# Optimization experiments

Hardware: AMD Instinct MI355X
Metric: run time of the kernel (lower is better)

Reference implementation:

```python
import jax, jax.numpy as jnp
import numpy as np

NUM_EXPERTS = 64
TOP_K = 8
NUM_TOKENS = 8192
HIDDEN = 1024
INTER = 512


def setup_inputs() -> dict:
    key = jax.random.key(0)
    k1, k2, k3, k4 = jax.random.split(key, 4)
    # 0.02 scale keeps activations in a sane range (randn weights with fan-in 1024)
    return {
        "hidden_states": jax.random.normal(k1, (NUM_TOKENS, HIDDEN), jnp.float32),
        "router_weight": jax.random.normal(k2, (HIDDEN, NUM_EXPERTS), jnp.float32) * 0.02,
        "merged_gate_up_proj": jax.random.normal(k3, (NUM_EXPERTS, HIDDEN, 2 * INTER), jnp.float32) * 0.02,
        "merged_down_proj": jax.random.normal(k4, (NUM_EXPERTS, INTER, HIDDEN), jnp.float32) * 0.02,
    }


def reference(hidden_states, router_weight, merged_gate_up_proj, merged_down_proj):
    T, H = hidden_states.shape
    E = router_weight.shape[1]

    # ---- Router: softmax over experts, top-k, renormalize top-k weights ----
    logits = hidden_states @ router_weight                       # [T, E]
    probs = jax.nn.softmax(logits, axis=-1)
    routing_weights, routing_indices = jax.lax.top_k(probs, TOP_K)  # [T, k]
    routing_weights = routing_weights / routing_weights.sum(-1, keepdims=True)

    # ---- Permute (haojun_permute_topk): replicate tokens topk times, stable-sort by expert ----
    flat_indices = routing_indices.reshape(-1)                   # [T*k]
    sort_order = jnp.argsort(flat_indices)                       # stable sort
    flat_states = jnp.repeat(hidden_states, TOP_K, axis=0)       # [T*k, H]
    permuted = flat_states[sort_order]                           # tokens grouped by expert
    group_sizes = jnp.bincount(flat_indices, length=E).astype(jnp.int32)  # tokens per expert

    # ---- Grouped MLP (grouped_gemm.gmm equivalent): y_i = x_i @ W[expert(i)] ----
    merged = jax.lax.ragged_dot(permuted, merged_gate_up_proj, group_sizes)  # [T*k, 2*I]
    gate, up = jnp.split(merged, 2, axis=-1)
    h = jax.nn.silu(gate) * up                                   # SiLU-gated (hidden_act='silu')
    expert_out = jax.lax.ragged_dot(h, merged_down_proj, group_sizes)        # [T*k, H]

    # ---- Unpermute: invert the sort, weight by routing probs, sum over top-k ----
    inv = jnp.argsort(sort_order)                                # unsort_order
    unpermuted = expert_out[inv].reshape(T, TOP_K, H)
    return (unpermuted * routing_weights[..., None]).sum(axis=1)  # [T, H]
```

## Files before the change

### kernel.cpp

```cpp
#include <hip/hip_runtime.h>
#include <cstdint>
#include <cstddef>

typedef __bf16 bf16_t;
typedef __bf16 bf16x8 __attribute__((ext_vector_type(8)));
typedef __bf16 bf16x4 __attribute__((ext_vector_type(4)));
typedef float f32x4 __attribute__((ext_vector_type(4)));

#define T_TOKENS 8192
#define HID 1024
#define INTER 512
#define NEXP 64
#define TOPK 8
#define NROWS (T_TOKENS * TOPK)
#define RT_TOK 16

typedef const unsigned int __attribute__((address_space(1)))* gptr_t;
typedef unsigned int __attribute__((address_space(3)))* lptr_t;

__device__ __forceinline__ void gload_lds16(const void* g, void* l) {
  __builtin_amdgcn_global_load_lds((gptr_t)g, (lptr_t)l, 16, 0, 0);
}

__device__ __forceinline__ f32x4 mfma16(bf16x8 a, bf16x8 b, f32x4 c) {
  return __builtin_amdgcn_mfma_f32_16x16x32_bf16(a, b, c, 0, 0, 0);
}

__device__ __forceinline__ int xcd_swizzle(int bid, int nwg) {
  int q = nwg >> 3;
  int xcd = bid & 7, i = bid >> 3;
  return xcd * q + i;
}

__global__ void transpose_cvt2_kernel(const float* __restrict__ w1, bf16_t* __restrict__ Wt1,
                                      const float* __restrict__ w2, bf16_t* __restrict__ Wt2,
                                      int* __restrict__ cntz) {
  const int tid = threadIdx.x;
  if (blockIdx.x == 0 && blockIdx.y == 0 && blockIdx.z == 0 && tid < 128) cntz[tid] = 0;

  const int e = blockIdx.z;
  const float* W; bf16_t* Wt; int K, k0;
  if (blockIdx.y < 16) {
    W = w1; Wt = Wt1; K = 1024; k0 = blockIdx.y * 64;
  } else {
    W = w2; Wt = Wt2; K = 512; k0 = (blockIdx.y - 16) * 64;
  }
  const int N = 1024;
  const int n0 = blockIdx.x * 64;

  __shared__ bf16_t tile[64][65];
  {
    const int r = tid >> 2, cq = tid & 3;
    const float* src = W + ((size_t)e * K + k0 + r) * N + n0 + cq * 16;
#pragma unroll
    for (int q = 0; q < 4; ++q) {
      float4 v = *(const float4*)(src + q * 4);
      tile[r][cq * 16 + q * 4 + 0] = (bf16_t)v.x;
      tile[r][cq * 16 + q * 4 + 1] = (bf16_t)v.y;
      tile[r][cq * 16 + q * 4 + 2] = (bf16_t)v.z;
      tile[r][cq * 16 + q * 4 + 3] = (bf16_t)v.w;
    }
  }
  __syncthreads();
  {
    const int nl = tid >> 2, kq = tid & 3;
    __align__(16) bf16_t tmp[16];
#pragma unroll
    for (int i = 0; i < 16; ++i) tmp[i] = tile[kq * 16 + i][nl];
    bf16_t* dst = Wt + ((size_t)e * N + n0 + nl) * K + k0 + kq * 16;
    *(bf16x8*)(dst + 0) = *(const bf16x8*)(tmp + 0);
    *(bf16x8*)(dst + 8) = *(const bf16x8*)(tmp + 8);
  }
}

__launch_bounds__(256, 2)
__global__ void router_kernel(const float* __restrict__ hs, const float* __restrict__ rw,
                              float* __restrict__ wval, int* __restrict__ widx,
                              bf16_t* __restrict__ hb) {
  const int t0 = blockIdx.x * RT_TOK;
  const int tid = threadIdx.x;
  const int lane = tid & 63, w = tid >> 6;
  __shared__ float hsl[RT_TOK][HID / 4][4];
  __shared__ float part[4][RT_TOK][NEXP];

  for (int i = tid; i < RT_TOK * (HID / 4); i += 256) {
    int t = i >> 8, c = i & 255;
    float4 v = ((const float4*)(hs + (size_t)(t0 + t) * HID))[c];
    *(float4*)&hsl[t][c][0] = v;
    bf16x4 o;
    o[0] = (bf16_t)v.x; o[1] = (bf16_t)v.y; o[2] = (bf16_t)v.z; o[3] = (bf16_t)v.w;
    *(bf16x4*)(hb + (size_t)(t0 + t) * HID + c * 4) = o;
  }
  __syncthreads();

  float acc[RT_TOK];
#pragma unroll
  for (int t = 0; t < RT_TOK; ++t) acc[t] = 0.f;
  const int kb = w * 256;
  for (int kc = 0; kc < 64; ++kc) {
    const int k = kb + kc * 4;
    float r0 = rw[(size_t)(k + 0) * NEXP + lane];
    float r1 = rw[(size_t)(k + 1) * NEXP + lane];
    float r2 = rw[(size_t)(k + 2) * NEXP + lane];
    float r3 = rw[(size_t)(k + 3) * NEXP + lane];
#pragma unroll
    for (int t = 0; t < RT_TOK; ++t) {
      float4 hv = *(const float4*)&hsl[t][(kb >> 2) + kc][0];
      acc[t] = fmaf(hv.x, r0, acc[t]);
      acc[t] = fmaf(hv.y, r1, acc[t]);
      acc[t] = fmaf(hv.z, r2, acc[t]);
      acc[t] = fmaf(hv.w, r3, acc[t]);
    }
  }
#pragma unroll
  for (int t = 0; t < RT_TOK; ++t) part[w][t][lane] = acc[t];
  __syncthreads();

  for (int j = 0; j < 4; ++j) {
    const int t = w * 4 + j;
    float logit = part[0][t][lane] + part[1][t][lane] + part[2][t][lane] + part[3][t][lane];
    float m = logit;
    for (int off = 32; off; off >>= 1) m = fmaxf(m, __shfl_xor(m, off));
    float ex = expf(logit - m);
    float Z = ex;
    for (int off = 32; off; off >>= 1) Z += __shfl_xor(Z, off);
    float p = ex / Z;
    float sum8 = 0.f;
    float outv[8]; int outi[8];
#pragma unroll
    for (int s = 0; s < 8; ++s) {
      float v = p; int idx = lane;
      for (int off = 32; off; off >>= 1) {
        float vv = __shfl_xor(v, off);
        int ii = __shfl_xor(idx, off);
        if (vv > v || (vv == v && ii < idx)) { v = vv; idx = ii; }
      }
      outv[s] = v; outi[s] = idx; sum8 += v;
      if (lane == idx) p = -1.f;
    }
    if (lane == 0) {
      float inv = 1.f / sum8;
#pragma unroll
      for (int s = 0; s < 8; ++s) {
        wval[(size_t)(t0 + t) * TOPK + s] = outv[s] * inv;
        widx[(size_t)(t0 + t) * TOPK + s] = outi[s];
      }
    }
  }
}

__global__ void hist_kernel(const int* __restrict__ widx, int* __restrict__ cnt) {
  __shared__ int h[NEXP];
  if (threadIdx.x < NEXP) h[threadIdx.x] = 0;
  __syncthreads();
  for (int i = blockIdx.x * blockDim.x + threadIdx.x; i < NROWS; i += gridDim.x * blockDim.x)
    atomicAdd(&h[widx[i]], 1);
  __syncthreads();
  if (threadIdx.x < NEXP) atomicAdd(&cnt[threadIdx.x], h[threadIdx.x]);
}

__global__ void assign_kernel(const int* __restrict__ widx, const int* __restrict__ cnt,
                              int* __restrict__ cnt2, int* __restrict__ row_org,
                              int* __restrict__ seg) {
  __shared__ int segl[NEXP];
  const int tid = threadIdx.x;
  if (tid < NEXP) {
    int a = 0;
    for (int j = 0; j < tid; ++j) a += cnt[j];
    segl[tid] = a;
    if (blockIdx.x == 0) {
      seg[tid] = a;
      if (tid == NEXP - 1) seg[NEXP] = a + cnt[NEXP - 1];
    }
  }
  __syncthreads();
  for (int i = blockIdx.x * blockDim.x + tid; i < NROWS; i += gridDim.x * blockDim.x) {
    int e = widx[i];
    int p = segl[e] + atomicAdd(&cnt2[e], 1);
    row_org[p] = i;
  }
}

__launch_bounds__(256, 2)
__global__ void gemm1_kernel(const bf16_t* __restrict__ hb, const bf16_t* __restrict__ Wt1,
                             const int* __restrict__ row_org, const int* __restrict__ seg,
                             bf16_t* __restrict__ h) {
  const int bid = blockIdx.x + gridDim.x * (blockIdx.y + gridDim.y * blockIdx.z);
  const int swz = xcd_swizzle(bid, 16 * 4 * NEXP);
  const int mt = swz & 15;
  const int nt = (swz >> 4) & 3;
  const int e = swz >> 6;

  const int ms = seg[e];
  const int sz = seg[e + 1] - ms;
  const int n0 = nt * 128;
  const int tid = threadIdx.x;
  const int lane = tid & 63;
  const int wid = tid >> 6;
  const int wm = wid >> 1, wn = wid & 1;
  __shared__ __align__(16) bf16_t As[128 * 64];
  __shared__ __align__(16) bf16_t Bs[256 * 64];

  const int srow = tid >> 3;
  const int cg = (tid & 7) ^ (srow & 7);

  size_t boff[8];
#pragma unroll
  for (int b = 0; b < 8; ++b) {
    int brow = b * 32 + srow;
    int n = (brow < 128) ? (n0 + brow) : (512 + n0 + (brow - 128));
    boff[b] = ((size_t)e * 1024 + n) * 1024 + cg * 8;
  }
  const int l15 = lane & 15, l4 = lane >> 4;

  for (int m0 = mt * 128; m0 < sz; m0 += 16 * 128) {
    size_t aoff[4];
#pragma unroll
    for (int a = 0; a < 4; ++a) {
      int row = a * 32 + srow;
      int idx = m0 + row; if (idx >= sz) idx = sz - 1;
      aoff[a] = (size_t)(row_org[ms + idx] >> 3) * HID + cg * 8;
    }
    f32x4 accg[4][4], accu[4][4];
#pragma unroll
    for (int mi = 0; mi < 4; ++mi)
#pragma unroll
      for (int ni = 0; ni < 4; ++ni) {
        accg[mi][ni] = (f32x4){0.f, 0.f, 0.f, 0.f};
        accu[mi][ni] = (f32x4){0.f, 0.f, 0.f, 0.f};
      }

    for (int kt = 0; kt < 16; ++kt) {
      const int ko = kt * 64;
      __syncthreads();
#pragma unroll
      for (int a = 0; a < 4; ++a)
        gload_lds16(hb + aoff[a] + ko, (char*)As + a * 4096 + tid * 16);
#pragma unroll
      for (int b = 0; b < 8; ++b)
        gload_lds16(Wt1 + boff[b] + ko, (char*)Bs + b * 4096 + tid * 16);
      __syncthreads();
#pragma unroll
      for (int kf = 0; kf < 2; ++kf) {
        const int ch = kf * 4 + l4;
        bf16x8 af[4], bg[4], bu[4];
#pragma unroll
        for (int mi = 0; mi < 4; ++mi) {
          int r = wm * 64 + mi * 16 + l15;
          af[mi] = *(const bf16x8*)((const char*)As + r * 128 + ((ch ^ (r & 7)) << 4));
        }
#pragma unroll
        for (int ni = 0; ni < 4; ++ni) {
          int rg = wn * 64 + ni * 16 + l15;
          bg[ni] = *(const bf16x8*)((const char*)Bs + rg * 128 + ((ch ^ (rg & 7)) << 4));
          int ru = rg + 128;
          bu[ni] = *(const bf16x8*)((const char*)Bs + ru * 128 + ((ch ^ (ru & 7)) << 4));
        }
#pragma unroll
        for (int mi = 0; mi < 4; ++mi)
#pragma unroll
          for (int ni = 0; ni < 4; ++ni) {
            accg[mi][ni] = mfma16(af[mi], bg[ni], accg[mi][ni]);
            accu[mi][ni] = mfma16(af[mi], bu[ni], accu[mi][ni]);
          }
      }
    }
#pragma unroll
    for (int mi = 0; mi < 4; ++mi) {
#pragma unroll
      for (int j = 0; j < 4; ++j) {
        int mrow = wm * 64 + mi * 16 + l4 * 4 + j;
        int idx = m0 + mrow;
        if (idx < sz) {
          bf16_t* hrow = h + (size_t)(ms + idx) * INTER + n0 + wn * 64 + l15;
#pragma unroll
          for (int ni = 0; ni < 4; ++ni) {
            float g = accg[mi][ni][j];
            float u = accu[mi][ni][j];
            float s = g / (1.f + __expf(-g));
            hrow[ni * 16] = (bf16_t)(s * u);
          }
        }
      }
    }
  }
}

__launch_bounds__(256, 2)
__global__ void gemm2_kernel(const bf16_t* __restrict__ h, const bf16_t* __restrict__ Wt2,
                             const int* __restrict__ row_org, const int* __restrict__ seg,
                             bf16_t* __restrict__ eo) {
  const int bid = blockIdx.x + gridDim.x * (blockIdx.y + gridDim.y * blockIdx.z);
  const int swz = xcd_swizzle(bid, 16 * 8 * NEXP);
  const int mt = swz & 15;
  const int nt = (swz >> 4) & 7;
  const int e = swz >> 7;

  const int ms = seg[e];
  const int sz = seg[e + 1] - ms;
  const int n0 = nt * 128;
  const int tid = threadIdx.x;
  const int lane = tid & 63;
  const int wid = tid >> 6;
  const int wm = wid >> 1, wn = wid & 1;
  __shared__ __align__(16) bf16_t As[128 * 64];
  __shared__ __align__(16) bf16_t Bs[128 * 64];
  const int srow = tid >> 3;
  const int cg = (tid & 7) ^ (srow & 7);
  size_t boff[4];
#pragma unroll
  for (int b = 0; b < 4; ++b) {
    int brow = b * 32 + srow;
    boff[b] = ((size_t)e * 1024 + n0 + brow) * INTER + cg * 8;
  }
  const int l15 = lane & 15, l4 = lane >> 4;

  for (int m0 = mt * 128; m0 < sz; m0 += 16 * 128) {
    size_t aoff[4];
#pragma unroll
    for (int a = 0; a < 4; ++a) {
      int row = a * 32 + srow;
      int idx = m0 + row; if (idx >= sz) idx = sz - 1;
      aoff[a] = (size_t)(ms + idx) * INTER + cg * 8;
    }
    f32x4 acc[4][4];
#pragma unroll
    for (int mi = 0; mi < 4; ++mi)
#pragma unroll
      for (int ni = 0; ni < 4; ++ni) acc[mi][ni] = (f32x4){0.f, 0.f, 0.f, 0.f};

    for (int kt = 0; kt < 8; ++kt) {
      const int ko = kt * 64;
      __syncthreads();
#pragma unroll
      for (int a = 0; a < 4; ++a)
        gload_lds16(h + aoff[a] + ko, (char*)As + a * 4096 + tid * 16);
#pragma unroll
      for (int b = 0; b < 4; ++b)
        gload_lds16(Wt2 + boff[b] + ko, (char*)Bs + b * 4096 + tid * 16);
      __syncthreads();
#pragma unroll
      for (int kf = 0; kf < 2; ++kf) {
        const int ch = kf * 4 + l4;
        bf16x8 af[4], bb[4];
#pragma unroll
        for (int mi = 0; mi < 4; ++mi) {
          int r = wm * 64 + mi * 16 + l15;
          af[mi] = *(const bf16x8*)((const char*)As + r * 128 + ((ch ^ (r & 7)) << 4));
        }
#pragma unroll
        for (int ni = 0; ni < 4; ++ni) {
          int r = wn * 64 + ni * 16 + l15;
          bb[ni] = *(const bf16x8*)((const char*)Bs + r * 128 + ((ch ^ (r & 7)) << 4));
        }
#pragma unroll
        for (int mi = 0; mi < 4; ++mi)
#pragma unroll
          for (int ni = 0; ni < 4; ++ni)
            acc[mi][ni] = mfma16(af[mi], bb[ni], acc[mi][ni]);
      }
    }
#pragma unroll
    for (int mi = 0; mi < 4; ++mi) {
#pragma unroll
      for (int j = 0; j < 4; ++j) {
        int mrow = wm * 64 + mi * 16 + l4 * 4 + j;
        int idx = m0 + mrow;
        if (idx < sz) {
          int org = row_org[ms + idx];
          bf16_t* orow = eo + (size_t)org * HID + n0 + wn * 64 + l15;
#pragma unroll
          for (int ni = 0; ni < 4; ++ni)
            orow[ni * 16] = (bf16_t)acc[mi][ni][j];
        }
      }
    }
  }
}

__global__ void unpermute_kernel(const bf16_t* __restrict__ eo, const float* __restrict__ wval,
                                 float* __restrict__ out) {
  const int t = blockIdx.x * 2 + (threadIdx.x >> 7);
  const int c0 = (threadIdx.x & 127) * 8;
  float w[8];
#pragma unroll
  for (int s = 0; s < 8; ++s) w[s] = wval[(size_t)t * 8 + s];
  float acc[8] = {0.f, 0.f, 0.f, 0.f, 0.f, 0.f, 0.f, 0.f};
#pragma unroll
  for (int s = 0; s < 8; ++s) {
    bf16x8 v = *(const bf16x8*)(eo + ((size_t)t * 8 + s) * HID + c0);
#pragma unroll
    for (int q = 0; q < 8; ++q) acc[q] = fmaf(w[s], (float)v[q], acc[q]);
  }
  *(float4*)(out + (size_t)t * HID + c0) = *(float4*)&acc[0];
  *(float4*)(out + (size_t)t * HID + c0 + 4) = *(float4*)&acc[4];
}

extern "C" void kernel_launch(void* const* d_in, const int* in_sizes, int n_in,
                              void* d_out, int out_size, void* d_ws, size_t ws_size,
                              hipStream_t stream) {
  (void)in_sizes; (void)n_in; (void)ws_size; (void)out_size;
  const float* hs = (const float*)d_in[0];
  const float* rw = (const float*)d_in[1];
  const float* w1 = (const float*)d_in[2];
  const float* w2 = (const float*)d_in[3];
  float* out = (float*)d_out;

  char* p = (char*)d_ws;
  size_t off = 0;
  auto carve = [&](size_t bytes) {
    void* r = p + off;
    off = (off + bytes + 255) & ~(size_t)255;
    return r;
  };
  bf16_t* Wt1  = (bf16_t*)carve((size_t)NEXP * 1024 * 1024 * 2);
  bf16_t* Wt2  = (bf16_t*)carve((size_t)NEXP * 1024 * 512 * 2);
  bf16_t* hb   = (bf16_t*)carve((size_t)T_TOKENS * HID * 2);
  bf16_t* hmid = (bf16_t*)carve((size_t)NROWS * INTER * 2);
  float* wval  = (float*)carve((size_t)NROWS * 4);
  int* widx    = (int*)carve((size_t)NROWS * 4);
  int* row_org = (int*)carve((size_t)NROWS * 4);
  int* cnt     = (int*)carve(512);
  int* seg     = (int*)carve(66 * 4);
  int* cnt2    = cnt + 64;

  bf16_t* eo = Wt1;

  transpose_cvt2_kernel<<<dim3(16, 24, 64), 256, 0, stream>>>(w1, Wt1, w2, Wt2, cnt);
  router_kernel<<<T_TOKENS / RT_TOK, 256, 0, stream>>>(hs, rw, wval, widx, hb);
  hist_kernel<<<128, 256, 0, stream>>>(widx, cnt);
  assign_kernel<<<128, 256, 0, stream>>>(widx, cnt, cnt2, row_org, seg);
  gemm1_kernel<<<dim3(16, 4, NEXP), 256, 0, stream>>>(hb, Wt1, row_org, seg, hmid);
  gemm2_kernel<<<dim3(16, 8, NEXP), 256, 0, stream>>>(hmid, Wt2, row_org, seg, eo);
  unpermute_kernel<<<T_TOKENS / 2, 256, 0, stream>>>(eo, wval, out);
}
```

Before: 600.0 us.

## Triple-buffer gemm1 LDS loads with 512-thread blocks and MFMA priority

Restructures the gate/up grouped GEMM to use 512-thread blocks (8 waves, 2x4 wave grid) and a 3-stage LDS ring, prefetching two k-tiles ahead with explicit vmcnt waits instead of a double __syncthreads per iteration. MFMA sections are wrapped with s_setprio to favor compute issue, and the M-tile grid is halved to 8 tiles per expert. The aim is to overlap global->LDS loads with MFMA work and cut barrier stalls. In exchange, LDS use grows to 144KB per block, allowing only one block per CU, and fewer blocks are launched.

```diff
diff --git a/kernel.cpp b/kernel.cpp
--- a/kernel.cpp
+++ b/kernel.cpp
@@ -181,15 +181,15 @@
   }
 }
 
-__launch_bounds__(256, 2)
+__launch_bounds__(512, 1)
 __global__ void gemm1_kernel(const bf16_t* __restrict__ hb, const bf16_t* __restrict__ Wt1,
                              const int* __restrict__ row_org, const int* __restrict__ seg,
                              bf16_t* __restrict__ h) {
   const int bid = blockIdx.x + gridDim.x * (blockIdx.y + gridDim.y * blockIdx.z);
-  const int swz = xcd_swizzle(bid, 16 * 4 * NEXP);
-  const int mt = swz & 15;
-  const int nt = (swz >> 4) & 3;
-  const int e = swz >> 6;
+  const int swz = xcd_swizzle(bid, 8 * 4 * NEXP);
+  const int mt = swz & 7;
+  const int nt = (swz >> 3) & 3;
+  const int e = swz >> 5;
 
   const int ms = seg[e];
   const int sz = seg[e + 1] - ms;
@@ -197,74 +197,98 @@
   const int tid = threadIdx.x;
   const int lane = tid & 63;
   const int wid = tid >> 6;
-  const int wm = wid >> 1, wn = wid & 1;
-  __shared__ __align__(16) bf16_t As[128 * 64];
-  __shared__ __align__(16) bf16_t Bs[256 * 64];
+  const int wm = wid >> 2;
+  const int wn = wid & 3;
+
+  __shared__ __align__(16) bf16_t As[3][128 * 64];
+  __shared__ __align__(16) bf16_t Bs[3][256 * 64];
 
   const int srow = tid >> 3;
   const int cg = (tid & 7) ^ (srow & 7);
 
-  size_t boff[8];
-#pragma unroll
-  for (int b = 0; b < 8; ++b) {
-    int brow = b * 32 + srow;
+  size_t boff[4];
+#pragma unroll
+  for (int b = 0; b < 4; ++b) {
+    int brow = b * 64 + srow;
     int n = (brow < 128) ? (n0 + brow) : (512 + n0 + (brow - 128));
     boff[b] = ((size_t)e * 1024 + n) * 1024 + cg * 8;
   }
   const int l15 = lane & 15, l4 = lane >> 4;
 
-  for (int m0 = mt * 128; m0 < sz; m0 += 16 * 128) {
-    size_t aoff[4];
-#pragma unroll
-    for (int a = 0; a < 4; ++a) {
-      int row = a * 32 + srow;
+  for (int m0 = mt * 128; m0 < sz; m0 += 8 * 128) {
+    size_t aoff[2];
+#pragma unroll
+    for (int a = 0; a < 2; ++a) {
+      int row = a * 64 + srow;
       int idx = m0 + row; if (idx >= sz) idx = sz - 1;
       aoff[a] = (size_t)(row_org[ms + idx] >> 3) * HID + cg * 8;
     }
-    f32x4 accg[4][4], accu[4][4];
+    f32x4 accg[4][2], accu[4][2];
 #pragma unroll
     for (int mi = 0; mi < 4; ++mi)
 #pragma unroll
-      for (int ni = 0; ni < 4; ++ni) {
-        accg[mi][ni] = (f32x4){0.f, 0.f, 0.f, 0.f};
-        accu[mi][ni] = (f32x4){0.f, 0.f, 0.f, 0.f};
-      }
+      for (int gi = 0; gi < 2; ++gi) {
+        accg[mi][gi] = (f32x4){0.f, 0.f, 0.f, 0.f};
+        accu[mi][gi] = (f32x4){0.f, 0.f, 0.f, 0.f};
+      }
+
+    auto stage = [&](int buf, int kt) {
+      const int ko = kt * 64;
+#pragma unroll
+      for (int a = 0; a < 2; ++a)
+        gload_lds16(hb + aoff[a] + ko, (char*)&As[buf][0] + a * 8192 + tid * 16);
+#pragma unroll
+      for (int b = 0; b < 4; ++b)
+        gload_lds16(Wt1 + boff[b] + ko, (char*)&Bs[buf][0] + b * 8192 + tid * 16);
+    };
+
+    stage(0, 0);
+    stage(1, 1);
+    asm volatile("s_waitcnt vmcnt(6)\n\ts_barrier" ::: "memory");
 
     for (int kt = 0; kt < 16; ++kt) {
-      const int ko = kt * 64;
-      __syncthreads();
-#pragma unroll
-      for (int a = 0; a < 4; ++a)
-        gload_lds16(hb + aoff[a] + ko, (char*)As + a * 4096 + tid * 16);
-#pragma unroll
-      for (int b = 0; b < 8; ++b)
-        gload_lds16(Wt1 + boff[b] + ko, (char*)Bs + b * 4096 + tid * 16);
-      __syncthreads();
-#pragma unroll
-      for (int kf = 0; kf < 2; ++kf) {
-        const int ch = kf * 4 + l4;
-        bf16x8 af[4], bg[4], bu[4];
-#pragma unroll
-        for (int mi = 0; mi < 4; ++mi) {
+      const int cur = kt % 3;
+      if (kt < 14) stage((kt + 2) % 3, kt + 2);
+      const char* Ab = (const char*)&As[cur][0];
+      const char* Bb = (const char*)&Bs[cur][0];
+      bf16x8 af[4][2], bg[2][2], bu[2][2];
+#pragma unroll
+      for (int mi = 0; mi < 4; ++mi)
+#pragma unroll
+        for (int kf = 0; kf < 2; ++kf) {
           int r = wm * 64 + mi * 16 + l15;
-          af[mi] = *(const bf16x8*)((const char*)As + r * 128 + ((ch ^ (r & 7)) << 4));
-        }
-#pragma unroll
-        for (int ni = 0; ni < 4; ++ni) {
-          int rg = wn * 64 + ni * 16 + l15;
-          bg[ni] = *(const bf16x8*)((const char*)Bs + rg * 128 + ((ch ^ (rg & 7)) << 4));
+          int ch = kf * 4 + l4;
+          af[mi][kf] = *(const bf16x8*)(Ab + r * 128 + ((ch ^ (r & 7)) << 4));
+        }
+#pragma unroll
+      for (int gi = 0; gi < 2; ++gi)
+#pragma unroll
+        for (int kf = 0; kf < 2; ++kf) {
+          int rg = wn * 32 + gi * 16 + l15;
+          int ch = kf * 4 + l4;
+          bg[gi][kf] = *(const bf16x8*)(Bb + rg * 128 + ((ch ^ (rg & 7)) << 4));
           int ru = rg + 128;
-          bu[ni] = *(const bf16x8*)((const char*)Bs + ru * 128 + ((ch ^ (ru & 7)) << 4));
-        }
-#pragma unroll
-        for (int mi = 0; mi < 4; ++mi)
-#pragma unroll
-          for (int ni = 0; ni < 4; ++ni) {
-            accg[mi][ni] = mfma16(af[mi], bg[ni], accg[mi][ni]);
-            accu[mi][ni] = mfma16(af[mi], bu[ni], accu[mi][ni]);
+          bu[gi][kf] = *(const bf16x8*)(Bb + ru * 128 + ((ch ^ (ru & 7)) << 4));
+        }
+      __builtin_amdgcn_s_setprio(1);
+#pragma unroll
+      for (int mi = 0; mi < 4; ++mi)
+#pragma unroll
+        for (int gi = 0; gi < 2; ++gi)
+#pragma unroll
+          for (int kf = 0; kf < 2; ++kf) {
+            accg[mi][gi] = mfma16(af[mi][kf], bg[gi][kf], accg[mi][gi]);
+            accu[mi][gi] = mfma16(af[mi][kf], bu[gi][kf], accu[mi][gi]);
           }
-      }
-    }
+      __builtin_amdgcn_s_setprio(0);
+      if (kt < 14) {
+        asm volatile("s_waitcnt vmcnt(6)\n\ts_barrier" ::: "memory");
+      } else if (kt == 14) {
+        asm volatile("s_waitcnt vmcnt(0)\n\ts_barrier" ::: "memory");
+      }
+    }
+    __syncthreads();
+
 #pragma unroll
     for (int mi = 0; mi < 4; ++mi) {
 #pragma unroll
@@ -272,13 +296,13 @@
         int mrow = wm * 64 + mi * 16 + l4 * 4 + j;
         int idx = m0 + mrow;
         if (idx < sz) {
-          bf16_t* hrow = h + (size_t)(ms + idx) * INTER + n0 + wn * 64 + l15;
-#pragma unroll
-          for (int ni = 0; ni < 4; ++ni) {
-            float g = accg[mi][ni][j];
-            float u = accu[mi][ni][j];
+          bf16_t* hrow = h + (size_t)(ms + idx) * INTER + n0 + wn * 32 + l15;
+#pragma unroll
+          for (int gi = 0; gi < 2; ++gi) {
+            float g = accg[mi][gi][j];
+            float u = accu[mi][gi][j];
             float s = g / (1.f + __expf(-g));
-            hrow[ni * 16] = (bf16_t)(s * u);
+            hrow[gi * 16] = (bf16_t)(s * u);
           }
         }
       }
@@ -430,7 +454,7 @@
   router_kernel<<<T_TOKENS / RT_TOK, 256, 0, stream>>>(hs, rw, wval, widx, hb);
   hist_kernel<<<128, 256, 0, stream>>>(widx, cnt);
   assign_kernel<<<128, 256, 0, stream>>>(widx, cnt, cnt2, row_org, seg);
-  gemm1_kernel<<<dim3(16, 4, NEXP), 256, 0, stream>>>(hb, Wt1, row_org, seg, hmid);
+  gemm1_kernel<<<dim3(8, 4, NEXP), 512, 0, stream>>>(hb, Wt1, row_org, seg, hmid);
   gemm2_kernel<<<dim3(16, 8, NEXP), 256, 0, stream>>>(hmid, Wt2, row_org, seg, eo);
   unpermute_kernel<<<T_TOKENS / 2, 256, 0, stream>>>(eo, wval, out);
 }
```

Result: slower. 713.6 us (+18.9%).
